# Kernel tuning notes

Hardware: AMD Instinct MI355X
Metric: run time of the kernel (lower is better)

Reference implementation:

```python
import jax, jax.numpy as jnp
import numpy as np
import math

H = 256  # hidden dim hardcoded in module; d_k = 256
EPS = 1e-5  # torch LayerNorm eps


def _mlp2(x, W1, b1, W2, b2):
    # nn.Sequential(Linear, Tanh, Linear, Tanh)
    return jnp.tanh(jnp.tanh(x @ W1 + b1) @ W2 + b2)


def _ln(x, w, b):
    mu = x.mean(-1, keepdims=True)
    var = ((x - mu) ** 2).mean(-1, keepdims=True)
    return (x - mu) / jnp.sqrt(var + EPS) * w + b


def setup_inputs():
    B, N, D, A = 128, 32, 128, 16
    key = jax.random.key(0)
    ks = jax.random.split(key, 32)

    def lin(k, i, o):
        return jax.random.normal(k, (i, o), jnp.float32) / np.sqrt(i).astype(np.float32)

    inp = {
        'states': jax.random.normal(ks[0], (B, N, D), jnp.float32),
        'policies': jax.nn.softmax(jax.random.normal(ks[1], (B, N, A), jnp.float32), axis=-1),
        'actions': jax.nn.one_hot(jax.random.randint(ks[2], (B, N), 0, A), A, dtype=jnp.float32),
    }
    # two-layer MLP params: state_embed(se), key(k), query(q), state_act_embed(sa),
    # attention_value(av), curr_agent_state_embed(ca)
    ins = {'se': D, 'k': H, 'q': H, 'sa': D + A, 'av': H, 'ca': D}
    i = 3
    for n in ['se', 'k', 'q', 'sa', 'av', 'ca']:
        inp[n + '_W1'] = lin(ks[i], ins[n], H); inp[n + '_b1'] = jnp.zeros((H,), jnp.float32)
        inp[n + '_W2'] = lin(ks[i + 1], H, H);  inp[n + '_b2'] = jnp.zeros((H,), jnp.float32)
        i += 2
    inp['f_W1'] = lin(ks[i], 2 * H, H); inp['f_b1'] = jnp.zeros((H,), jnp.float32); i += 1
    inp['f_W2'] = lin(ks[i], H, H);     inp['f_b2'] = jnp.zeros((H,), jnp.float32); i += 1
    inp['f_W3'] = lin(ks[i], H, A);     inp['f_b3'] = jnp.zeros((A,), jnp.float32); i += 1
    inp['ln1_w'] = jnp.ones((H,), jnp.float32); inp['ln1_b'] = jnp.zeros((H,), jnp.float32)
    inp['ln2_w'] = jnp.ones((H,), jnp.float32); inp['ln2_b'] = jnp.zeros((H,), jnp.float32)
    return inp


def reference(states, policies, actions,
              se_W1, se_b1, se_W2, se_b2,
              k_W1, k_b1, k_W2, k_b2,
              q_W1, q_b1, q_W2, q_b2,
              sa_W1, sa_b1, sa_W2, sa_b2,
              av_W1, av_b1, av_W2, av_b2,
              ca_W1, ca_b1, ca_W2, ca_b2,
              f_W1, f_b1, f_W2, f_b2, f_W3, f_b3,
              ln1_w, ln1_b, ln2_w, ln2_b):
    B, N, D = states.shape
    # remove_self_loops: per-agent gather of all other agents (static index map)
    nbr = np.array([[j for j in range(N) if j != i] for i in range(N)])  # [N, N-1]
    states_key = states[:, nbr, :]        # [B,N,N-1,D]
    actions_nb = actions[:, nbr, :]       # [B,N,N-1,A]
    obs_actions = jnp.concatenate([states_key, actions_nb], axis=-1)

    sq_embed = _mlp2(states, se_W1, se_b1, se_W2, se_b2)       # [B,N,256] (query path)
    sk_embed = _mlp2(states_key, se_W1, se_b1, se_W2, se_b2)   # [B,N,N-1,256]
    key_obs = _mlp2(sk_embed, k_W1, k_b1, k_W2, k_b2)          # [B,N,N-1,256]
    query_obs = _mlp2(sq_embed, q_W1, q_b1, q_W2, q_b2)        # [B,N,256]

    scores = jnp.einsum('bnd,bnmd->bnm', query_obs, key_obs) / math.sqrt(float(H))
    weight = jax.nn.softmax(scores, axis=-1)                   # [B,N,N-1]

    # weight_assignment: insert 1.0 at the self position
    rows = np.arange(N)[:, None]
    weights_full = jnp.zeros((B, N, N), weight.dtype).at[:, rows, nbr].set(weight)
    weights_full = weights_full.at[:, np.arange(N), np.arange(N)].set(1.0)

    oa_embed = _mlp2(obs_actions, sa_W1, sa_b1, sa_W2, sa_b2)  # [B,N,N-1,256]
    att_vals = _mlp2(oa_embed, av_W1, av_b1, av_W2, av_b2)     # [B,N,N-1,256]
    node_feat = jnp.einsum('bnm,bnmd->bnd', weight, att_vals)  # [B,N,256]
    node_feat = _ln(oa_embed.mean(axis=-2) + node_feat, ln1_w, ln1_b)

    cur = _mlp2(states, ca_W1, ca_b1, ca_W2, ca_b2)
    cur = _ln(cur + sk_embed.mean(axis=-2) + sq_embed, ln2_w, ln2_b)

    feat = jnp.concatenate([cur, node_feat], axis=-1)          # [B,N,512]
    h = jnp.tanh(feat @ f_W1 + f_b1)
    h = jnp.tanh(h @ f_W2 + f_b2)
    Q = h @ f_W3 + f_b3                                        # [B,N,A]

    Value = jnp.einsum('bna,bma->bnm', Q, policies)            # Q @ policies^T -> [B,N,N]
    Q_value = jnp.sum(actions * Q, axis=-1, keepdims=True)     # [B,N,1]
    return Value, Q_value, weights_full
```

## Files before the change

### kernel.cpp

```cpp
#include <hip/hip_runtime.h>
#include <hip/hip_bf16.h>


struct Ptrs37 { const void* p[37]; };
struct Meta37 { int sz[37]; unsigned off[37]; };

typedef __attribute__((ext_vector_type(8))) short bf16x8;
typedef __attribute__((ext_vector_type(4))) float f32x4;

__device__ __forceinline__ bool is_bf16_env(const void* ln1w) {
  return (*(const unsigned int*)ln1w) != 0x3f800000u;
}
__device__ __forceinline__ unsigned short f2bf(float f) {
  union { __hip_bfloat16 h; unsigned short u; } cv;
  cv.h = __float2bfloat16(f);
  return cv.u;
}

__global__ __launch_bounds__(256) void convert_inputs_kernel(Ptrs37 ptrs, Meta37 meta, float* F) {
  int i = blockIdx.y;
  int n = meta.sz[i];
  bool bf = is_bf16_env(ptrs.p[33]);
  float* dst = F + meta.off[i];
  if (bf) {
    const unsigned short* s = (const unsigned short*)ptrs.p[i];
    for (int idx = blockIdx.x * 256 + threadIdx.x; idx < n; idx += gridDim.x * 256) {
      unsigned int u = ((unsigned int)s[idx]) << 16;
      dst[idx] = __uint_as_float(u);
    }
  } else {
    const float* s = (const float*)ptrs.p[i];
    for (int idx = blockIdx.x * 256 + threadIdx.x; idx < n; idx += gridDim.x * 256)
      dst[idx] = s[idx];
  }
}

struct PrepW { unsigned srcOff[14]; unsigned dstOff[14]; int K[14]; int Kp[14]; };
__global__ __launch_bounds__(256) void prep_w_kernel(PrepW pw, const float* __restrict__ F,
                                                     unsigned short* __restrict__ WT) {
  int m = blockIdx.y;
  const float* src = F + pw.srcOff[m];
  unsigned short* dst = WT + pw.dstOff[m];
  int K = pw.K[m], Kp = pw.Kp[m];
  int total = 256 * Kp;
  for (int idx = blockIdx.x * 256 + threadIdx.x; idx < total; idx += gridDim.x * 256) {
    int n = idx / Kp, k = idx - n * Kp;
    dst[idx] = (k < K) ? f2bf(src[(size_t)k * 256 + n]) : (unsigned short)0;
  }
}

__global__ __launch_bounds__(256) void concat_kernel(const float* __restrict__ S,
                                                     const float* __restrict__ A,
                                                     float* __restrict__ OAin) {
  int gid = blockIdx.x * 256 + threadIdx.x;
  if (gid >= 4096 * 160) return;
  int r = gid / 160;
  int c = gid - r * 160;
  float v = 0.f;
  if (c < 128) v = S[r * 128 + c];
  else if (c < 144) v = A[r * 16 + (c - 128)];
  OAin[gid] = v;
}

struct GemmDesc { const float* X; const unsigned short* WT; const float* bias; float* Y; int K; };
struct GemmStage { GemmDesc g[3]; };

__global__ __launch_bounds__(256) void gemm_mfma_kernel(GemmStage st) {
  GemmDesc d = st.g[blockIdx.z];
  const float* __restrict__ X = d.X;
  const unsigned short* __restrict__ WT = d.WT;
  const float* __restrict__ Bv = d.bias;
  float* __restrict__ Y = d.Y;
  const int K = d.K;
  __shared__ uint4 AsB[256];
  __shared__ uint4 BsB[256];
  const int tid = threadIdx.x;
  const int l = tid & 63, w = tid >> 6;
  const int m0 = blockIdx.y << 6, n0 = blockIdx.x << 6;
  const int wm = w >> 1, wn = w & 1;
  const int arow = wm * 32 + (l & 15);
  const int brow = wn * 32 + (l & 15);
  const int koff = (l >> 4) * 8;
  const float* ax = X + (size_t)(m0 + (tid >> 2)) * K + (tid & 3) * 8;
  const unsigned short* bg = WT + (size_t)(n0 + (tid >> 2)) * K + (tid & 3) * 8;
  f32x4 acc[2][2] = {};
  for (int k0 = 0; k0 < K; k0 += 32) {
    float4 t0 = *(const float4*)(ax + k0);
    float4 t1 = *(const float4*)(ax + k0 + 4);
    uint4 bv = *(const uint4*)(bg + k0);
    unsigned short as8[8];
    as8[0] = f2bf(t0.x); as8[1] = f2bf(t0.y); as8[2] = f2bf(t0.z); as8[3] = f2bf(t0.w);
    as8[4] = f2bf(t1.x); as8[5] = f2bf(t1.y); as8[6] = f2bf(t1.z); as8[7] = f2bf(t1.w);
    __syncthreads();
    AsB[tid] = *(const uint4*)as8;
    BsB[tid] = bv;
    __syncthreads();
    const char* Ab = (const char*)AsB;
    const char* Bb = (const char*)BsB;
    bf16x8 a0 = *(const bf16x8*)(Ab + arow * 64 + koff * 2);
    bf16x8 a1 = *(const bf16x8*)(Ab + (arow + 16) * 64 + koff * 2);
    bf16x8 b0 = *(const bf16x8*)(Bb + brow * 64 + koff * 2);
    bf16x8 b1 = *(const bf16x8*)(Bb + (brow + 16) * 64 + koff * 2);
    acc[0][0] = __builtin_amdgcn_mfma_f32_16x16x32_bf16(a0, b0, acc[0][0], 0, 0, 0);
    acc[0][1] = __builtin_amdgcn_mfma_f32_16x16x32_bf16(a0, b1, acc[0][1], 0, 0, 0);
    acc[1][0] = __builtin_amdgcn_mfma_f32_16x16x32_bf16(a1, b0, acc[1][0], 0, 0, 0);
    acc[1][1] = __builtin_amdgcn_mfma_f32_16x16x32_bf16(a1, b1, acc[1][1], 0, 0, 0);
  }
  const int col0 = n0 + wn * 32 + (l & 15);
  const int rbase = m0 + wm * 32 + (l >> 4) * 4;
#pragma unroll
  for (int ni = 0; ni < 2; ++ni) {
    int col = col0 + ni * 16;
    float bias = Bv[col];
#pragma unroll
    for (int mi = 0; mi < 2; ++mi) {
#pragma unroll
      for (int r = 0; r < 4; ++r) {
        int row = rbase + mi * 16 + r;
        Y[(size_t)row * 256 + col] = tanhf(acc[mi][ni][r] + bias);
      }
    }
  }
}

__global__ __launch_bounds__(256) void attn_kernel(
    const float* __restrict__ Qb, const float* __restrict__ Kb,
    const float* __restrict__ AVp, const float* __restrict__ OAp,
    const float* __restrict__ SEp,
    float* __restrict__ NF, float* __restrict__ sumOA, float* __restrict__ sumSE,
    void* __restrict__ dout, const void* __restrict__ ln1w) {
  const size_t WF_OFF = 135168;
  int b = blockIdx.x;
  int tid = threadIdx.x;
  bool bf = is_bf16_env(ln1w);
  __shared__ float AVs[32 * 260];
  __shared__ float wsT[32][36];

  const float* avg = AVp + (size_t)b * 8192;
  for (int i = tid * 4; i < 8192; i += 1024) {
    int j = i >> 8, c = i & 255;
    *(float4*)&AVs[j * 260 + c] = *(const float4*)(avg + i);
  }
  {
    int c = tid;
    float sa = 0.f, ss = 0.f;
    const float* oab = OAp + (size_t)b * 8192 + c;
    const float* seb = SEp + (size_t)b * 8192 + c;
#pragma unroll 4
    for (int j = 0; j < 32; ++j) { sa += oab[j * 256]; ss += seb[j * 256]; }
    sumOA[b * 256 + c] = sa;
    sumSE[b * 256 + c] = ss;
  }

  int l = tid & 63, w = tid >> 6;
  int j = l & 31, h = l >> 5;
  const float* kbase = Kb + (size_t)b * 8192 + j * 256 + h * 128;
  const float* qbase = Qb + (size_t)b * 8192 + h * 128;
  for (int q = 0; q < 2; ++q) {
    int n0 = w * 8 + q * 4;
    float acc0 = 0.f, acc1 = 0.f, acc2 = 0.f, acc3 = 0.f;
    for (int t = 0; t < 32; ++t) {
      float4 kv = *(const float4*)(kbase + t * 4);
      float4 q0 = *(const float4*)(qbase + (n0 + 0) * 256 + t * 4);
      float4 q1 = *(const float4*)(qbase + (n0 + 1) * 256 + t * 4);
      float4 q2 = *(const float4*)(qbase + (n0 + 2) * 256 + t * 4);
      float4 q3 = *(const float4*)(qbase + (n0 + 3) * 256 + t * 4);
      acc0 += q0.x * kv.x + q0.y * kv.y + q0.z * kv.z + q0.w * kv.w;
      acc1 += q1.x * kv.x + q1.y * kv.y + q1.z * kv.z + q1.w * kv.w;
      acc2 += q2.x * kv.x + q2.y * kv.y + q2.z * kv.z + q2.w * kv.w;
      acc3 += q3.x * kv.x + q3.y * kv.y + q3.z * kv.z + q3.w * kv.w;
    }
#pragma unroll
    for (int i = 0; i < 4; ++i) {
      float part = (i == 0) ? acc0 : (i == 1) ? acc1 : (i == 2) ? acc2 : acc3;
      float full = part + __shfl_down(part, 32);
      int n = n0 + i;
      float sc = full * 0.0625f;
      if (j == n) sc = -1e30f;
      float mx = sc;
      mx = fmaxf(mx, __shfl_xor(mx, 16));
      mx = fmaxf(mx, __shfl_xor(mx, 8));
      mx = fmaxf(mx, __shfl_xor(mx, 4));
      mx = fmaxf(mx, __shfl_xor(mx, 2));
      mx = fmaxf(mx, __shfl_xor(mx, 1));
      float e = __expf(sc - mx);
      float s = e;
      s += __shfl_xor(s, 16); s += __shfl_xor(s, 8); s += __shfl_xor(s, 4);
      s += __shfl_xor(s, 2);  s += __shfl_xor(s, 1);
      float wgt = e / s;
      if (l < 32) {
        wsT[j][n] = wgt;
        size_t oi = WF_OFF + ((size_t)(b * 32 + n)) * 32 + j;
        float ov = (j == n) ? 1.0f : wgt;
        if (bf) ((__hip_bfloat16*)dout)[oi] = __float2bfloat16(ov);
        else    ((float*)dout)[oi] = ov;
      }
    }
  }
  __syncthreads();

  int tx = tid & 63, tyy = tid >> 6;
  float accn[8][4] = {};
  for (int jj = 0; jj < 32; ++jj) {
    float4 av = *(const float4*)&AVs[jj * 260 + (tx << 2)];
    const float* wr = &wsT[jj][tyy * 8];
#pragma unroll
    for (int g = 0; g < 8; ++g) {
      float wv = wr[g];
      accn[g][0] += av.x * wv; accn[g][1] += av.y * wv;
      accn[g][2] += av.z * wv; accn[g][3] += av.w * wv;
    }
  }
#pragma unroll
  for (int g = 0; g < 8; ++g) {
    float4 o = make_float4(accn[g][0], accn[g][1], accn[g][2], accn[g][3]);
    *(float4*)&NF[((size_t)(b * 32 + tyy * 8 + g)) * 256 + (tx << 2)] = o;
  }
}

__global__ __launch_bounds__(64) void ln_kernel(
    const float* __restrict__ NF, const float* __restrict__ sOA, const float* __restrict__ OAp,
    const float* __restrict__ Cc, const float* __restrict__ sSE, const float* __restrict__ SEp,
    const float* __restrict__ w1, const float* __restrict__ b1,
    const float* __restrict__ w2, const float* __restrict__ b2,
    float* __restrict__ feat) {
  int row = blockIdx.x, b = row >> 5, l = threadIdx.x;
  float x[4], y[4];
#pragma unroll
  for (int i = 0; i < 4; ++i) {
    int c = l + (i << 6);
    float oa = OAp[row * 256 + c];
    float se = SEp[row * 256 + c];
    x[i] = NF[row * 256 + c] + (sOA[b * 256 + c] - oa) * (1.0f / 31.0f);
    y[i] = Cc[row * 256 + c] + (sSE[b * 256 + c] - se) * (1.0f / 31.0f) + se;
  }
  float sx = x[0] + x[1] + x[2] + x[3];
  float sy = y[0] + y[1] + y[2] + y[3];
  for (int d = 1; d < 64; d <<= 1) { sx += __shfl_xor(sx, d); sy += __shfl_xor(sy, d); }
  float mx = sx * (1.0f / 256.0f), my = sy * (1.0f / 256.0f);
  float vx = 0.f, vy = 0.f;
#pragma unroll
  for (int i = 0; i < 4; ++i) {
    float dx = x[i] - mx; vx += dx * dx;
    float dy = y[i] - my; vy += dy * dy;
  }
  for (int d = 1; d < 64; d <<= 1) { vx += __shfl_xor(vx, d); vy += __shfl_xor(vy, d); }
  float rx = rsqrtf(vx * (1.0f / 256.0f) + 1e-5f);
  float ry = rsqrtf(vy * (1.0f / 256.0f) + 1e-5f);
#pragma unroll
  for (int i = 0; i < 4; ++i) {
    int c = l + (i << 6);
    feat[(size_t)row * 512 + 256 + c] = (x[i] - mx) * rx * w1[c] + b1[c];
    feat[(size_t)row * 512 + c]       = (y[i] - my) * ry * w2[c] + b2[c];
  }
}

__global__ __launch_bounds__(256) void qf_kernel(const float* __restrict__ H2,
                                                 const float* __restrict__ W3,
                                                 const float* __restrict__ b3,
                                                 float* __restrict__ QF) {
  int gid = blockIdx.x * 256 + threadIdx.x;
  int row = gid >> 4, a = gid & 15;
  const float* hp = H2 + (size_t)row * 256;
  float acc = b3[a];
#pragma unroll 8
  for (int k = 0; k < 256; ++k) acc += hp[k] * W3[k * 16 + a];
  QF[gid] = acc;
}

__global__ __launch_bounds__(256) void final_kernel(const float* __restrict__ QF,
                                                    const float* __restrict__ POL,
                                                    const float* __restrict__ ACT,
                                                    void* __restrict__ dout,
                                                    const void* __restrict__ ln1w) {
  bool bf = is_bf16_env(ln1w);
  int b = blockIdx.x, tid = threadIdx.x;
  __shared__ float qfs[512], pols[512], acts[512];
  for (int i = tid; i < 512; i += 256) {
    qfs[i]  = QF[(size_t)b * 512 + i];
    pols[i] = POL[(size_t)b * 512 + i];
    acts[i] = ACT[(size_t)b * 512 + i];
  }
  __syncthreads();
#pragma unroll
  for (int r = 0; r < 4; ++r) {
    int p = tid + (r << 8);
    int n = p >> 5, m = p & 31;
    float acc = 0.f;
#pragma unroll
    for (int a = 0; a < 16; ++a) acc += qfs[n * 16 + a] * pols[m * 16 + a];
    size_t oi = (size_t)b * 1024 + p;
    if (bf) ((__hip_bfloat16*)dout)[oi] = __float2bfloat16(acc);
    else    ((float*)dout)[oi] = acc;
  }
  if (tid < 32) {
    float acc = 0.f;
#pragma unroll
    for (int a = 0; a < 16; ++a) acc += acts[tid * 16 + a] * qfs[tid * 16 + a];
    size_t oi = 131072 + (size_t)b * 32 + tid;
    if (bf) ((__hip_bfloat16*)dout)[oi] = __float2bfloat16(acc);
    else    ((float*)dout)[oi] = acc;
  }
}

extern "C" void kernel_launch(void* const* d_in, const int* in_sizes, int n_in,
                              void* d_out, int out_size, void* d_ws, size_t ws_size,
                              hipStream_t stream) {
  (void)n_in; (void)out_size; (void)ws_size;
  Ptrs37 P; Meta37 M;
  unsigned off = 0;
  for (int i = 0; i < 37; ++i) {
    P.p[i] = d_in[i];
    M.sz[i] = in_sizes[i];
    M.off[i] = off;
    off += (unsigned)in_sizes[i];
  }
  float* F = (float*)d_ws;
  const unsigned MEG = 1048576u;
  unsigned X0 = (off + 511u) & ~511u;
  float* SE   = F + X0 + 0 * MEG;
  float* QB   = F + X0 + 1 * MEG;
  float* KB   = F + X0 + 2 * MEG;
  float* OA   = F + X0 + 3 * MEG;
  float* AV   = F + X0 + 4 * MEG;
  float* CC   = F + X0 + 5 * MEG;
  float* T1   = F + X0 + 6 * MEG;
  float* T2   = F + X0 + 7 * MEG;
  float* T3   = F + X0 + 8 * MEG;
  float* NF   = F + X0 + 9 * MEG;
  float* FEAT = F + X0 + 10 * MEG;
  float* OAIN = F + X0 + 12 * MEG;
  float* H1   = F + X0 + 13 * MEG;
  float* H2   = F + X0 + 14 * MEG;
  float* SOA  = F + X0 + 15 * MEG;
  float* SSE  = SOA + 32768;
  float* QFp  = SOA + 65536;
  unsigned short* WT = (unsigned short*)(F + X0 + 16 * MEG);
  auto Wp = [&](int i) { return F + M.off[i]; };
  const void* ln1w_raw = d_in[33];
  const float* ST = F + M.off[0];

  static const int wIdx[14] = {3,5,7,9,11,13,15,17,19,21,23,25,27,29};
  PrepW pw{};
  unsigned wtOff[37] = {};
  int Kp_[37] = {};
  unsigned cum = 0;
  for (int t = 0; t < 14; ++t) {
    int i = wIdx[t];
    int K = in_sizes[i] / 256;
    int Kp = (K + 31) & ~31;
    pw.srcOff[t] = M.off[i];
    pw.dstOff[t] = cum;
    pw.K[t] = K; pw.Kp[t] = Kp;
    wtOff[i] = cum; Kp_[i] = Kp;
    cum += (unsigned)(256 * Kp);
  }

  convert_inputs_kernel<<<dim3(128, 37), 256, 0, stream>>>(P, M, F);
  prep_w_kernel<<<dim3(32, 14), 256, 0, stream>>>(pw, F, WT);
  concat_kernel<<<(4096 * 160 + 255) / 256, 256, 0, stream>>>(ST, F + M.off[2], OAIN);

  auto G = [&](const float* X, int wi, int bi, float* Y) {
    GemmDesc g; g.X = X; g.WT = WT + wtOff[wi]; g.bias = Wp(bi); g.Y = Y; g.K = Kp_[wi];
    return g;
  };
  dim3 gg3(4, 64, 3), gg1(4, 64, 1);
  GemmStage s1{{ G(ST, 3, 4, T1),  G(OAIN, 15, 16, T2), G(ST, 23, 24, T3) }};
  gemm_mfma_kernel<<<gg3, 256, 0, stream>>>(s1);
  GemmStage s2{{ G(T1, 5, 6, SE),  G(T2, 17, 18, OA),  G(T3, 25, 26, CC) }};
  gemm_mfma_kernel<<<gg3, 256, 0, stream>>>(s2);
  GemmStage s3{{ G(SE, 7, 8, T1),  G(SE, 11, 12, T2),  G(OA, 19, 20, T3) }};
  gemm_mfma_kernel<<<gg3, 256, 0, stream>>>(s3);
  GemmStage s4{{ G(T1, 9, 10, KB), G(T2, 13, 14, QB), G(T3, 21, 22, AV) }};
  gemm_mfma_kernel<<<gg3, 256, 0, stream>>>(s4);

  attn_kernel<<<128, 256, 0, stream>>>(QB, KB, AV, OA, SE, NF, SOA, SSE, d_out, ln1w_raw);
  ln_kernel<<<4096, 64, 0, stream>>>(NF, SOA, OA, CC, SSE, SE,
                                     Wp(33), Wp(34), Wp(35), Wp(36), FEAT);

  GemmDesc g5 = G(FEAT, 27, 28, H1);
  GemmStage s5{{ g5, g5, g5 }};
  gemm_mfma_kernel<<<gg1, 256, 0, stream>>>(s5);
  GemmDesc g6 = G(H1, 29, 30, H2);
  GemmStage s6{{ g6, g6, g6 }};
  gemm_mfma_kernel<<<gg1, 256, 0, stream>>>(s6);

  qf_kernel<<<256, 256, 0, stream>>>(H2, Wp(31), Wp(32), QFp);
  final_kernel<<<128, 256, 0, stream>>>(QFp, F + M.off[1], F + M.off[2], d_out, ln1w_raw);
}
```

Before: 258.6 us.

## Merge prep kernels, double-buffer GEMM LDS, fuse Q head into final kernel

After: 256.1 us. Within noise of the previous version (-1.0%).

```diff
diff --git a/kernel.cpp b/kernel.cpp
--- a/kernel.cpp
+++ b/kernel.cpp
@@ -4,6 +4,7 @@
 
 struct Ptrs37 { const void* p[37]; };
 struct Meta37 { int sz[37]; unsigned off[37]; };
+struct PrepW  { int widx[14]; unsigned dstOff[14]; int K[14]; int Kp[14]; };
 
 typedef __attribute__((ext_vector_type(8))) short bf16x8;
 typedef __attribute__((ext_vector_type(4))) float f32x4;
@@ -17,49 +18,58 @@
   return cv.u;
 }
 
-__global__ __launch_bounds__(256) void convert_inputs_kernel(Ptrs37 ptrs, Meta37 meta, float* F) {
-  int i = blockIdx.y;
-  int n = meta.sz[i];
-  bool bf = is_bf16_env(ptrs.p[33]);
-  float* dst = F + meta.off[i];
-  if (bf) {
-    const unsigned short* s = (const unsigned short*)ptrs.p[i];
-    for (int idx = blockIdx.x * 256 + threadIdx.x; idx < n; idx += gridDim.x * 256) {
-      unsigned int u = ((unsigned int)s[idx]) << 16;
-      dst[idx] = __uint_as_float(u);
+__global__ __launch_bounds__(256) void prep_all_kernel(Ptrs37 P, Meta37 M, PrepW pw,
+                                                       float* __restrict__ F,
+                                                       unsigned short* __restrict__ WT,
+                                                       float* __restrict__ OAin) {
+  bool bf = is_bf16_env(P.p[33]);
+  int y = blockIdx.y;
+  int stride = gridDim.x * 256;
+  int g0 = blockIdx.x * 256 + threadIdx.x;
+  if (y < 37) {
+    int n = M.sz[y];
+    float* dst = F + M.off[y];
+    if (bf) {
+      const unsigned short* s = (const unsigned short*)P.p[y];
+      for (int idx = g0; idx < n; idx += stride)
+        dst[idx] = __uint_as_float(((unsigned int)s[idx]) << 16);
+    } else {
+      const float* s = (const float*)P.p[y];
+      for (int idx = g0; idx < n; idx += stride) dst[idx] = s[idx];
+    }
+  } else if (y < 51) {
+    int t = y - 37;
+    const void* src = P.p[pw.widx[t]];
+    unsigned short* dst = WT + pw.dstOff[t];
+    int K = pw.K[t], Kp = pw.Kp[t];
+    int total = 256 * Kp;
+    for (int idx = g0; idx < total; idx += stride) {
+      int n = idx / Kp, k = idx - n * Kp;
+      unsigned short v = 0;
+      if (k < K) {
+        size_t si = (size_t)k * 256 + n;
+        v = bf ? ((const unsigned short*)src)[si] : f2bf(((const float*)src)[si]);
+      }
+      dst[idx] = v;
     }
   } else {
-    const float* s = (const float*)ptrs.p[i];
-    for (int idx = blockIdx.x * 256 + threadIdx.x; idx < n; idx += gridDim.x * 256)
-      dst[idx] = s[idx];
-  }
-}
-
-struct PrepW { unsigned srcOff[14]; unsigned dstOff[14]; int K[14]; int Kp[14]; };
-__global__ __launch_bounds__(256) void prep_w_kernel(PrepW pw, const float* __restrict__ F,
-                                                     unsigned short* __restrict__ WT) {
-  int m = blockIdx.y;
-  const float* src = F + pw.srcOff[m];
-  unsigned short* dst = WT + pw.dstOff[m];
-  int K = pw.K[m], Kp = pw.Kp[m];
-  int total = 256 * Kp;
-  for (int idx = blockIdx.x * 256 + threadIdx.x; idx < total; idx += gridDim.x * 256) {
-    int n = idx / Kp, k = idx - n * Kp;
-    dst[idx] = (k < K) ? f2bf(src[(size_t)k * 256 + n]) : (unsigned short)0;
-  }
-}
-
-__global__ __launch_bounds__(256) void concat_kernel(const float* __restrict__ S,
-                                                     const float* __restrict__ A,
-                                                     float* __restrict__ OAin) {
-  int gid = blockIdx.x * 256 + threadIdx.x;
-  if (gid >= 4096 * 160) return;
-  int r = gid / 160;
-  int c = gid - r * 160;
-  float v = 0.f;
-  if (c < 128) v = S[r * 128 + c];
-  else if (c < 144) v = A[r * 16 + (c - 128)];
-  OAin[gid] = v;
+    const void* S = P.p[0];
+    const void* A = P.p[2];
+    for (int gid = g0; gid < 4096 * 160; gid += stride) {
+      int r = gid / 160, c = gid - r * 160;
+      float v = 0.f;
+      if (c < 128) {
+        size_t si = (size_t)r * 128 + c;
+        v = bf ? __uint_as_float(((unsigned int)((const unsigned short*)S)[si]) << 16)
+               : ((const float*)S)[si];
+      } else if (c < 144) {
+        size_t si = (size_t)r * 16 + (c - 128);
+        v = bf ? __uint_as_float(((unsigned int)((const unsigned short*)A)[si]) << 16)
+               : ((const float*)A)[si];
+      }
+      OAin[gid] = v;
+    }
+  }
 }
 
 struct GemmDesc { const float* X; const unsigned short* WT; const float* bias; float* Y; int K; };
@@ -72,8 +82,8 @@
   const float* __restrict__ Bv = d.bias;
   float* __restrict__ Y = d.Y;
   const int K = d.K;
-  __shared__ uint4 AsB[256];
-  __shared__ uint4 BsB[256];
+  __shared__ uint4 AsB[2][256];
+  __shared__ uint4 BsB[2][256];
   const int tid = threadIdx.x;
   const int l = tid & 63, w = tid >> 6;
   const int m0 = blockIdx.y << 6, n0 = blockIdx.x << 6;
@@ -84,19 +94,28 @@
   const float* ax = X + (size_t)(m0 + (tid >> 2)) * K + (tid & 3) * 8;
   const unsigned short* bg = WT + (size_t)(n0 + (tid >> 2)) * K + (tid & 3) * 8;
   f32x4 acc[2][2] = {};
-  for (int k0 = 0; k0 < K; k0 += 32) {
-    float4 t0 = *(const float4*)(ax + k0);
-    float4 t1 = *(const float4*)(ax + k0 + 4);
-    uint4 bv = *(const uint4*)(bg + k0);
+  {
+    float4 t0 = *(const float4*)ax;
+    float4 t1 = *(const float4*)(ax + 4);
+    uint4 bv = *(const uint4*)bg;
     unsigned short as8[8];
     as8[0] = f2bf(t0.x); as8[1] = f2bf(t0.y); as8[2] = f2bf(t0.z); as8[3] = f2bf(t0.w);
     as8[4] = f2bf(t1.x); as8[5] = f2bf(t1.y); as8[6] = f2bf(t1.z); as8[7] = f2bf(t1.w);
-    __syncthreads();
-    AsB[tid] = *(const uint4*)as8;
-    BsB[tid] = bv;
-    __syncthreads();
-    const char* Ab = (const char*)AsB;
-    const char* Bb = (const char*)BsB;
+    AsB[0][tid] = *(const uint4*)as8;
+    BsB[0][tid] = bv;
+  }
+  __syncthreads();
+  int cur = 0;
+  for (int k0 = 0; k0 < K; k0 += 32) {
+    const bool more = (k0 + 32) < K;
+    float4 n0f, n1f; uint4 nb;
+    if (more) {
+      n0f = *(const float4*)(ax + k0 + 32);
+      n1f = *(const float4*)(ax + k0 + 36);
+      nb  = *(const uint4*)(bg + k0 + 32);
+    }
+    const char* Ab = (const char*)AsB[cur];
+    const char* Bb = (const char*)BsB[cur];
     bf16x8 a0 = *(const bf16x8*)(Ab + arow * 64 + koff * 2);
     bf16x8 a1 = *(const bf16x8*)(Ab + (arow + 16) * 64 + koff * 2);
     bf16x8 b0 = *(const bf16x8*)(Bb + brow * 64 + koff * 2);
@@ -105,6 +124,15 @@
     acc[0][1] = __builtin_amdgcn_mfma_f32_16x16x32_bf16(a0, b1, acc[0][1], 0, 0, 0);
     acc[1][0] = __builtin_amdgcn_mfma_f32_16x16x32_bf16(a1, b0, acc[1][0], 0, 0, 0);
     acc[1][1] = __builtin_amdgcn_mfma_f32_16x16x32_bf16(a1, b1, acc[1][1], 0, 0, 0);
+    if (more) {
+      unsigned short as8[8];
+      as8[0] = f2bf(n0f.x); as8[1] = f2bf(n0f.y); as8[2] = f2bf(n0f.z); as8[3] = f2bf(n0f.w);
+      as8[4] = f2bf(n1f.x); as8[5] = f2bf(n1f.y); as8[6] = f2bf(n1f.z); as8[7] = f2bf(n1f.w);
+      AsB[cur ^ 1][tid] = *(const uint4*)as8;
+      BsB[cur ^ 1][tid] = nb;
+      __syncthreads();
+      cur ^= 1;
+    }
   }
   const int col0 = n0 + wn * 32 + (l & 15);
   const int rbase = m0 + wm * 32 + (l >> 4) * 4;
@@ -255,31 +283,41 @@
   }
 }
 
-__global__ __launch_bounds__(256) void qf_kernel(const float* __restrict__ H2,
-                                                 const float* __restrict__ W3,
-                                                 const float* __restrict__ b3,
-                                                 float* __restrict__ QF) {
-  int gid = blockIdx.x * 256 + threadIdx.x;
-  int row = gid >> 4, a = gid & 15;
-  const float* hp = H2 + (size_t)row * 256;
-  float acc = b3[a];
-#pragma unroll 8
-  for (int k = 0; k < 256; ++k) acc += hp[k] * W3[k * 16 + a];
-  QF[gid] = acc;
-}
-
-__global__ __launch_bounds__(256) void final_kernel(const float* __restrict__ QF,
-                                                    const float* __restrict__ POL,
-                                                    const float* __restrict__ ACT,
-                                                    void* __restrict__ dout,
-                                                    const void* __restrict__ ln1w) {
+__global__ __launch_bounds__(256) void qfinal_kernel(const float* __restrict__ H2,
+                                                     const float* __restrict__ W3,
+                                                     const float* __restrict__ b3,
+                                                     const float* __restrict__ POL,
+                                                     const float* __restrict__ ACT,
+                                                     void* __restrict__ dout,
+                                                     const void* __restrict__ ln1w) {
   bool bf = is_bf16_env(ln1w);
   int b = blockIdx.x, tid = threadIdx.x;
+  __shared__ float h2s[32 * 256];
+  __shared__ float w3s[256 * 16];
   __shared__ float qfs[512], pols[512], acts[512];
+  {
+    const float4* src = (const float4*)(H2 + (size_t)b * 8192);
+    float4* dst = (float4*)h2s;
+#pragma unroll
+    for (int i = 0; i < 8; ++i) dst[tid + i * 256] = src[tid + i * 256];
+    const float4* wsrc = (const float4*)W3;
+    float4* wdst = (float4*)w3s;
+#pragma unroll
+    for (int i = 0; i < 4; ++i) wdst[tid + i * 256] = wsrc[tid + i * 256];
+  }
   for (int i = tid; i < 512; i += 256) {
-    qfs[i]  = QF[(size_t)b * 512 + i];
     pols[i] = POL[(size_t)b * 512 + i];
     acts[i] = ACT[(size_t)b * 512 + i];
+  }
+  __syncthreads();
+#pragma unroll
+  for (int t = 0; t < 2; ++t) {
+    int p = tid + t * 256;
+    int row = p >> 4, a = p & 15;
+    float acc = b3[a];
+#pragma unroll 8
+    for (int k = 0; k < 256; ++k) acc += h2s[row * 256 + k] * w3s[k * 16 + a];
+    qfs[p] = acc;
   }
   __syncthreads();
 #pragma unroll
@@ -334,7 +372,6 @@
   float* H2   = F + X0 + 14 * MEG;
   float* SOA  = F + X0 + 15 * MEG;
   float* SSE  = SOA + 32768;
-  float* QFp  = SOA + 65536;
   unsigned short* WT = (unsigned short*)(F + X0 + 16 * MEG);
   auto Wp = [&](int i) { return F + M.off[i]; };
   const void* ln1w_raw = d_in[33];
@@ -349,16 +386,14 @@
     int i = wIdx[t];
     int K = in_sizes[i] / 256;
     int Kp = (K + 31) & ~31;
-    pw.srcOff[t] = M.off[i];
+    pw.widx[t] = i;
     pw.dstOff[t] = cum;
     pw.K[t] = K; pw.Kp[t] = Kp;
     wtOff[i] = cum; Kp_[i] = Kp;
     cum += (unsigned)(256 * Kp);
   }
 
-  convert_inputs_kernel<<<dim3(128, 37), 256, 0, stream>>>(P, M, F);
-  prep_w_kernel<<<dim3(32, 14), 256, 0, stream>>>(pw, F, WT);
-  concat_kernel<<<(4096 * 160 + 255) / 256, 256, 0, stream>>>(ST, F + M.off[2], OAIN);
+  prep_all_kernel<<<dim3(64, 52), 256, 0, stream>>>(P, M, pw, F, WT, OAIN);
 
   auto G = [&](const float* X, int wi, int bi, float* Y) {
     GemmDesc g; g.X = X; g.WT = WT + wtOff[wi]; g.bias = Wp(bi); g.Y = Y; g.K = Kp_[wi];
@@ -385,6 +420,6 @@
   GemmStage s6{{ g6, g6, g6 }};
   gemm_mfma_kernel<<<gg1, 256, 0, stream>>>(s6);
 
-  qf_kernel<<<256, 256, 0, stream>>>(H2, Wp(31), Wp(32), QFp);
-  final_kernel<<<128, 256, 0, stream>>>(QFp, F + M.off[1], F + M.off[2], d_out, ln1w_raw);
-}
+  qfinal_kernel<<<128, 256, 0, stream>>>(H2, Wp(31), Wp(32),
+                                         F + M.off[1], F + M.off[2], d_out, ln1w_raw);
+}
```
